# Optimization experiments

Measured on AMD Instinct MI355X. Metric: run time of the kernel, lower is better.

The kernel has to match this reference:

```python
import jax, jax.numpy as jnp
import numpy as np

SR = 44100
SHORT_TAU_MS = 50.0
LONG_TAU_MS = 3000.0


def ms2coef(ms, sr):
    return float(1.0 - np.exp(-2200.0 / (ms * sr)))


C_SHORT = ms2coef(SHORT_TAU_MS, SR)
C_LONG = ms2coef(LONG_TAU_MS, SR)
ALIGN_SHIFT = int(SR * (LONG_TAU_MS - SHORT_TAU_MS) * 0.0005)  # 65047


def _ema(x, coef):
    """One-pole EMA along last axis: y[t] = coef*x[t] + (1-coef)*y[t-1], y[-1]=0.
    Implemented as a parallel (associative) scan over the linear recurrence."""
    a = jnp.full_like(x, 1.0 - coef)
    b = coef * x

    def combine(l, r):
        a1, b1 = l
        a2, b2 = r
        return (a1 * a2, a2 * b1 + b2)

    _, y = jax.lax.associative_scan(combine, (a, b), axis=-1)
    return y


def _ldr(x):
    # flatten leading dims, then log(short EMA) - log(rolled long EMA)
    x = x.reshape(-1, x.shape[-1])
    short = _ema(x, C_SHORT)
    long_ = jnp.roll(_ema(x, C_LONG), -ALIGN_SHIFT, axis=-1)
    return jnp.log(short) - jnp.log(long_)


def setup_inputs() -> dict:
    key = jax.random.key(0)
    k1, k2 = jax.random.split(key)
    B, T = 16, 1048576
    # squared signals: strictly positive (tiny offset avoids log(0) at t=0)
    pred_sq = jax.random.uniform(k1, (B, T), dtype=jnp.float32) + 1e-6
    target_sq = jax.random.uniform(k2, (B, T), dtype=jnp.float32) + 1e-6
    return {"pred_sq": pred_sq, "target_sq": target_sq}


def reference(pred_sq, target_sq):
    return jnp.mean(jnp.abs(_ldr(pred_sq) - _ldr(target_sq)))
```

## Files before the change

kernel.cpp:

```cpp
#include <hip/hip_runtime.h>
#include <math.h>

#define TPB   256
#define SL    16
#define SEGS  65536
#define TLEN  1048576
#define MOFF  4065
#define ROFF  7
#define NEMA  4
#define TPL   256

typedef float v4f __attribute__((ext_vector_type(4)));

__device__ __forceinline__ float comp(const float4& v, int m) {
    return m == 0 ? v.x : m == 1 ? v.y : m == 2 ? v.z : v.w;
}

__device__ __forceinline__ float ipowf(float base, int e) {
    float r = 1.0f, p = base;
    while (e) { if (e & 1) r *= p; p *= p; e >>= 1; }
    return r;
}

__global__ __launch_bounds__(TPB) void ldr_partials(
    const float* __restrict__ pred, const float* __restrict__ targ,
    float amS, float amL, float Ac16S, float Ac16L,
    float* __restrict__ pB, float* __restrict__ tA, int rows)
{
    __shared__ float wt[4][NEMA];
    const int bgl = blockIdx.x;
    const int r = bgl >> 8, tile = bgl & 255;
    const int j = threadIdx.x, lane = j & 63, w = j >> 6;
    const int m = tile * 256 + j;
    const size_t base = (size_t)r * TLEN + (size_t)m * SL;
    const float* P = pred + base;
    const float* T = targ + base;

    v4f u0, u1, u2, u3, w0, w1, w2, w3;
    asm volatile(
        "global_load_dwordx4 %[u0], %[pa], off\n\t"
        "global_load_dwordx4 %[u1], %[pa], off offset:16\n\t"
        "global_load_dwordx4 %[u2], %[pa], off offset:32\n\t"
        "global_load_dwordx4 %[u3], %[pa], off offset:48\n\t"
        "global_load_dwordx4 %[w0], %[ta], off\n\t"
        "global_load_dwordx4 %[w1], %[ta], off offset:16\n\t"
        "global_load_dwordx4 %[w2], %[ta], off offset:32\n\t"
        "global_load_dwordx4 %[w3], %[ta], off offset:48\n\t"
        "s_waitcnt vmcnt(0)"
        : [u0] "=&v"(u0), [u1] "=&v"(u1), [u2] "=&v"(u2), [u3] "=&v"(u3),
          [w0] "=&v"(w0), [w1] "=&v"(w1), [w2] "=&v"(w2), [w3] "=&v"(w3)
        : [pa] "v"(P), [ta] "v"(T)
        : "memory");

    float sp = 0.f, st = 0.f, lp = 0.f, lt = 0.f;
    #define PQ(Q) { sp = fmaf(amS, sp, Q.x); lp = fmaf(amL, lp, Q.x);         \
                    sp = fmaf(amS, sp, Q.y); lp = fmaf(amL, lp, Q.y);         \
                    sp = fmaf(amS, sp, Q.z); lp = fmaf(amL, lp, Q.z);         \
                    sp = fmaf(amS, sp, Q.w); lp = fmaf(amL, lp, Q.w); }
    #define TQ(Q) { st = fmaf(amS, st, Q.x); lt = fmaf(amL, lt, Q.x);         \
                    st = fmaf(amS, st, Q.y); lt = fmaf(amL, lt, Q.y);         \
                    st = fmaf(amS, st, Q.z); lt = fmaf(amL, lt, Q.z);         \
                    st = fmaf(amS, st, Q.w); lt = fmaf(amL, lt, Q.w); }
    PQ(u0) PQ(u1) PQ(u2) PQ(u3)
    TQ(w0) TQ(w1) TQ(w2) TQ(w3)
    #undef PQ
    #undef TQ

    const size_t plane = (size_t)rows * SEGS;
    const size_t idx = (size_t)r * SEGS + m;
    pB[0 * plane + idx] = sp;
    pB[1 * plane + idx] = st;
    pB[2 * plane + idx] = lp;
    pB[3 * plane + idx] = lt;

    const float wgtS = ipowf(Ac16S, 63 - lane);
    const float wgtL = ipowf(Ac16L, 63 - lane);
    float vals[NEMA] = { sp * wgtS, st * wgtS, lp * wgtL, lt * wgtL };
    #pragma unroll
    for (int E = 0; E < NEMA; ++E) {
        float s = vals[E];
        #pragma unroll
        for (int d = 32; d > 0; d >>= 1) s += __shfl_xor(s, d, 64);
        if (lane == 0) wt[w][E] = s;
    }
    __syncthreads();
    if (j == 0) {
        const float A64S = ipowf(Ac16S, 64), A64L = ipowf(Ac16L, 64);
        #pragma unroll
        for (int E = 0; E < NEMA; ++E) {
            const float A64 = (E < 2) ? A64S : A64L;
            float t = wt[0][E];
            t = fmaf(A64, t, wt[1][E]);
            t = fmaf(A64, t, wt[2][E]);
            t = fmaf(A64, t, wt[3][E]);
            tA[((size_t)E * rows + r) * TPL + tile] = t;
        }
    }
}

__global__ __launch_bounds__(64) void ldr_tile_scan(
    const float* __restrict__ tA, float* __restrict__ tC,
    float AcT_S, float AcT_L, int rows)
{
    const int g = blockIdx.x, lane = threadIdx.x;
    const float AcT = (g < 2 * rows) ? AcT_S : AcT_L;
    const float AcT4 = ((AcT * AcT) * (AcT * AcT));
    const float* Bv = tA + (size_t)g * TPL + lane * 4;
    float b4[4];
    float B = 0.f;
    #pragma unroll
    for (int m = 0; m < 4; ++m) { b4[m] = Bv[m]; B = fmaf(AcT, B, b4[m]); }
    float incl = B, Ad = AcT4;
    #pragma unroll
    for (int d = 1; d < 64; d <<= 1) {
        float pb = __shfl_up(incl, d, 64);
        if (lane >= d) incl = fmaf(Ad, pb, incl);
        Ad *= Ad;
    }
    float carry = __shfl_up(incl, 1, 64);
    if (lane == 0) carry = 0.f;
    float* co = tC + (size_t)g * TPL + lane * 4;
    #pragma unroll
    for (int m = 0; m < 4; ++m) {
        co[m] = carry;
        carry = fmaf(AcT, carry, b4[m]);
    }
}

__global__ __launch_bounds__(TPB) void ldr_loss(
    const float* __restrict__ pred, const float* __restrict__ targ,
    const float* __restrict__ pB, const float* __restrict__ tC,
    float amS, float amL, float Ac16S, float Ac16L,
    float* __restrict__ partial, int rows)
{
    __shared__ float sS[2][4], sL[2][4];
    __shared__ float longC[2][512];
    __shared__ float rs[4];
    const int bgl = blockIdx.x;
    const int r = bgl >> 8, bl = bgl & 255;
    const int j = threadIdx.x, lane = j & 63, w = j >> 6;
    const int m = bl * 256 + j;
    const size_t plane = (size_t)rows * SEGS;
    const size_t rbase = (size_t)r * SEGS;

    const float A1024S = ipowf(Ac16S, 64);
    const float aLaneS = ipowf(Ac16S, lane);
    float aggS[2];
    aggS[0] = pB[0 * plane + rbase + m];
    aggS[1] = pB[1 * plane + rbase + m];
    float inS0 = aggS[0], inS1 = aggS[1], Ad = Ac16S;
    #pragma unroll
    for (int d = 1; d < 64; d <<= 1) {
        float p0 = __shfl_up(inS0, d, 64);
        float p1 = __shfl_up(inS1, d, 64);
        if (lane >= d) { inS0 = fmaf(Ad, p0, inS0); inS1 = fmaf(Ad, p1, inS1); }
        Ad *= Ad;
    }
    float exS0 = __shfl_up(inS0, 1, 64), exS1 = __shfl_up(inS1, 1, 64);
    if (lane == 0) { exS0 = 0.f; exS1 = 0.f; }
    if (lane == 63) { sS[0][w] = inS0; sS[1][w] = inS1; }

    const int half = j >> 7;
    const int hh = j & 127;
    const int tsel = (bl + 15 + half) & 255;
    const float Ac32L = Ac16L * Ac16L;
    const float A2048L = ipowf(Ac32L, 64);
    const float aLaneL = ipowf(Ac32L, lane);
    float2 agL0 = *(const float2*)(pB + 2 * plane + rbase + tsel * 256 + 2 * hh);
    float2 agL1 = *(const float2*)(pB + 3 * plane + rbase + tsel * 256 + 2 * hh);
    float pa0 = fmaf(Ac16L, agL0.x, agL0.y);
    float pa1 = fmaf(Ac16L, agL1.x, agL1.y);
    float inL0 = pa0, inL1 = pa1;
    Ad = Ac32L;
    #pragma unroll
    for (int d = 1; d < 64; d <<= 1) {
        float p0 = __shfl_up(inL0, d, 64);
        float p1 = __shfl_up(inL1, d, 64);
        if (lane >= d) { inL0 = fmaf(Ad, p0, inL0); inL1 = fmaf(Ad, p1, inL1); }
        Ad *= Ad;
    }
    float exL0 = __shfl_up(inL0, 1, 64), exL1 = __shfl_up(inL1, 1, 64);
    if (lane == 0) { exL0 = 0.f; exL1 = 0.f; }
    if (lane == 63) { sL[0][w] = inL0; sL[1][w] = inL1; }
    __syncthreads();

    {
        const float baseS0 = tC[((size_t)0 * rows + r) * TPL + bl];
        const float baseS1 = tC[((size_t)1 * rows + r) * TPL + bl];
        float Wc0 = 0.f, Wc1 = 0.f;
        for (int u = 0; u < w; ++u) {
            Wc0 = fmaf(Wc0, A1024S, sS[0][u]);
            Wc1 = fmaf(Wc1, A1024S, sS[1][u]);
        }
        const float aThS = aLaneS * ipowf(A1024S, w);
        exS0 = fmaf(aThS, baseS0, fmaf(aLaneS, Wc0, exS0));
        exS1 = fmaf(aThS, baseS1, fmaf(aLaneS, Wc1, exS1));
    }
    {
        const float baseL0 = tC[((size_t)2 * rows + r) * TPL + tsel];
        const float baseL1 = tC[((size_t)3 * rows + r) * TPL + tsel];
        const int hw = w & 1, fw = w & 2;
        float Wc0 = hw ? sL[0][fw] : 0.f;
        float Wc1 = hw ? sL[1][fw] : 0.f;
        const float aThL = aLaneL * (hw ? A2048L : 1.f);
        float c00 = fmaf(aThL, baseL0, fmaf(aLaneL, Wc0, exL0));
        float c10 = fmaf(aThL, baseL1, fmaf(aLaneL, Wc1, exL1));
        const int i0 = half * 256 + 2 * hh;
        longC[0][i0] = c00; longC[0][i0 + 1] = fmaf(Ac16L, c00, agL0.x);
        longC[1][i0] = c10; longC[1][i0 + 1] = fmaf(Ac16L, c10, agL1.x);
    }
    __syncthreads();
    const float cSp = exS0, cSt = exS1;
    const float cLp = longC[0][225 + j];
    const float cLt = longC[1][225 + j];

    const int a = (m + MOFF) & (SEGS - 1);
    const int bseg = (m + MOFF + 1) & (SEGS - 1);
    const float* P = pred + (size_t)r * TLEN;
    const float* T = targ + (size_t)r * TLEN;

    float sp[SL], st[SL];
    {
        const float4* Sp4 = (const float4*)(P + (size_t)m * SL);
        const float4* St4 = (const float4*)(T + (size_t)m * SL);
        float ysp = cSp, yst = cSt;
        #pragma unroll
        for (int q = 0; q < SL / 4; ++q) {
            float4 u = Sp4[q], v = St4[q];
            #pragma unroll
            for (int mm = 0; mm < 4; ++mm) {
                ysp = fmaf(amS, ysp, comp(u, mm)); sp[4 * q + mm] = ysp;
                yst = fmaf(amS, yst, comp(v, mm)); st[4 * q + mm] = yst;
            }
        }
    }
    float ylp = cLp, ylt = cLt;
    const float4* Ap4 = (const float4*)(P + (size_t)a * SL);
    const float4* At4 = (const float4*)(T + (size_t)a * SL);
    const float4* Bp4 = (const float4*)(P + (size_t)bseg * SL);
    const float4* Bt4 = (const float4*)(T + (size_t)bseg * SL);

    float lsum = 0.f;
    #pragma unroll
    for (int q = 0; q < SL / 4; ++q) {
        float4 u = Ap4[q], v = At4[q];
        #pragma unroll
        for (int mm = 0; mm < 4; ++mm) {
            const int e = 4 * q + mm;
            ylp = fmaf(amL, ylp, comp(u, mm));
            ylt = fmaf(amL, ylt, comp(v, mm));
            if (e >= ROFF) {
                const int i = e - ROFF;
                lsum += fabsf(__logf(__fdividef(sp[i] * ylt, st[i] * ylp)));
            }
        }
    }
    #pragma unroll
    for (int q = 0; q < 2; ++q) {
        float4 u = Bp4[q], v = Bt4[q];
        #pragma unroll
        for (int mm = 0; mm < 4; ++mm) {
            const int e = 4 * q + mm;
            if (e < ROFF) {
                ylp = fmaf(amL, ylp, comp(u, mm));
                ylt = fmaf(amL, ylt, comp(v, mm));
                const int i = e + (SL - ROFF);
                lsum += fabsf(__logf(__fdividef(sp[i] * ylt, st[i] * ylp)));
            }
        }
    }

    #pragma unroll
    for (int d = 32; d > 0; d >>= 1) lsum += __shfl_xor(lsum, d, 64);
    if (lane == 0) rs[w] = lsum;
    __syncthreads();
    if (j == 0) partial[bgl] = rs[0] + rs[1] + rs[2] + rs[3];
}

__global__ void ldr_finalize(const float* __restrict__ partial, int nparts,
                             float* __restrict__ out, double inv_n)
{
    __shared__ double sd[256];
    double s = 0.0;
    for (int i = threadIdx.x; i < nparts; i += 256) s += (double)partial[i];
    sd[threadIdx.x] = s;
    __syncthreads();
    for (int d = 128; d > 0; d >>= 1) {
        if (threadIdx.x < d) sd[threadIdx.x] += sd[threadIdx.x + d];
        __syncthreads();
    }
    if (threadIdx.x == 0) out[0] = (float)(sd[0] * inv_n);
}

extern "C" void kernel_launch(void* const* d_in, const int* in_sizes, int n_in,
                              void* d_out, int out_size, void* d_ws, size_t ws_size,
                              hipStream_t stream)
{
    const float* pred = (const float*)d_in[0];
    const float* targ = (const float*)d_in[1];
    const int n = in_sizes[0];
    const int rows = n / TLEN;

    const double csd = 1.0 - exp(-2200.0 / (50.0 * 44100.0));
    const double cld = 1.0 - exp(-2200.0 / (3000.0 * 44100.0));
    const double amSd = 1.0 - csd, amLd = 1.0 - cld;
    const float amS = (float)amSd, amL = (float)amLd;
    const float Ac16S = (float)pow(amSd, 16.0);
    const float Ac16L = (float)pow(amLd, 16.0);
    const float AcT_S = (float)pow(amSd, 4096.0);
    const float AcT_L = (float)pow(amLd, 4096.0);

    char* wsb = (char*)d_ws;
    float* pB      = (float*)(wsb + 256);
    float* tA      = pB + (size_t)NEMA * rows * SEGS;
    float* tC      = tA + (size_t)NEMA * rows * TPL;
    float* partial = tC + (size_t)NEMA * rows * TPL;

    const int nblocks = rows * TPL;
    const int nplanes = NEMA * rows;

    ldr_partials<<<nblocks, TPB, 0, stream>>>(pred, targ, amS, amL,
                                              Ac16S, Ac16L, pB, tA, rows);
    ldr_tile_scan<<<nplanes, 64, 0, stream>>>(tA, tC, AcT_S, AcT_L, rows);
    ldr_loss<<<nblocks, TPB, 0, stream>>>(pred, targ, pB, tC, amS, amL,
                                          Ac16S, Ac16L, partial, rows);

    const double inv_n = 1.0 / ((double)rows * (double)TLEN);
    ldr_finalize<<<1, 256, 0, stream>>>(partial, nblocks, (float*)d_out, inv_n);
}
```

Baseline: 75.51 us.

## Fuse tile scan into loss kernel and recompute short-EMA partials locally

Removes the separate tile-scan launch: each wave of every loss block redundantly scans one of the four 256-entry tile-aggregate planes and picks out the carries it needs. Short-EMA segment partials are no longer stored by the first kernel. The loss kernel instead recomputes them from its own segment loads, which it already needed, now issued up front with inline asm. This saves one launch, the scan kernel's traffic and half the partial-plane writes and reads. In exchange every block repeats the small tile scans and holds 32 more live registers across the scan phase.

```diff
diff --git a/kernel.cpp b/kernel.cpp
--- a/kernel.cpp
+++ b/kernel.cpp
@@ -7,7 +7,6 @@
 #define TLEN  1048576
 #define MOFF  4065
 #define ROFF  7
-#define NEMA  4
 #define TPL   256
 
 typedef float v4f __attribute__((ext_vector_type(4)));
@@ -22,12 +21,28 @@
     return r;
 }
 
+#define LOAD8(P, T, U0,U1,U2,U3, W0,W1,W2,W3)                                 \
+    asm volatile(                                                             \
+        "global_load_dwordx4 %[u0], %[pa], off\n\t"                           \
+        "global_load_dwordx4 %[u1], %[pa], off offset:16\n\t"                 \
+        "global_load_dwordx4 %[u2], %[pa], off offset:32\n\t"                 \
+        "global_load_dwordx4 %[u3], %[pa], off offset:48\n\t"                 \
+        "global_load_dwordx4 %[w0], %[ta], off\n\t"                           \
+        "global_load_dwordx4 %[w1], %[ta], off offset:16\n\t"                 \
+        "global_load_dwordx4 %[w2], %[ta], off offset:32\n\t"                 \
+        "global_load_dwordx4 %[w3], %[ta], off offset:48\n\t"                 \
+        "s_waitcnt vmcnt(0)"                                                  \
+        : [u0] "=&v"(U0), [u1] "=&v"(U1), [u2] "=&v"(U2), [u3] "=&v"(U3),     \
+          [w0] "=&v"(W0), [w1] "=&v"(W1), [w2] "=&v"(W2), [w3] "=&v"(W3)      \
+        : [pa] "v"(P), [ta] "v"(T)                                            \
+        : "memory")
+
 __global__ __launch_bounds__(TPB) void ldr_partials(
     const float* __restrict__ pred, const float* __restrict__ targ,
     float amS, float amL, float Ac16S, float Ac16L,
-    float* __restrict__ pB, float* __restrict__ tA, int rows)
+    float* __restrict__ pBL, float* __restrict__ tA, int rows)
 {
-    __shared__ float wt[4][NEMA];
+    __shared__ float wt[4][4];
     const int bgl = blockIdx.x;
     const int r = bgl >> 8, tile = bgl & 255;
     const int j = threadIdx.x, lane = j & 63, w = j >> 6;
@@ -37,20 +52,7 @@
     const float* T = targ + base;
 
     v4f u0, u1, u2, u3, w0, w1, w2, w3;
-    asm volatile(
-        "global_load_dwordx4 %[u0], %[pa], off\n\t"
-        "global_load_dwordx4 %[u1], %[pa], off offset:16\n\t"
-        "global_load_dwordx4 %[u2], %[pa], off offset:32\n\t"
-        "global_load_dwordx4 %[u3], %[pa], off offset:48\n\t"
-        "global_load_dwordx4 %[w0], %[ta], off\n\t"
-        "global_load_dwordx4 %[w1], %[ta], off offset:16\n\t"
-        "global_load_dwordx4 %[w2], %[ta], off offset:32\n\t"
-        "global_load_dwordx4 %[w3], %[ta], off offset:48\n\t"
-        "s_waitcnt vmcnt(0)"
-        : [u0] "=&v"(u0), [u1] "=&v"(u1), [u2] "=&v"(u2), [u3] "=&v"(u3),
-          [w0] "=&v"(w0), [w1] "=&v"(w1), [w2] "=&v"(w2), [w3] "=&v"(w3)
-        : [pa] "v"(P), [ta] "v"(T)
-        : "memory");
+    LOAD8(P, T, u0, u1, u2, u3, w0, w1, w2, w3);
 
     float sp = 0.f, st = 0.f, lp = 0.f, lt = 0.f;
     #define PQ(Q) { sp = fmaf(amS, sp, Q.x); lp = fmaf(amL, lp, Q.x);         \
@@ -68,16 +70,14 @@
 
     const size_t plane = (size_t)rows * SEGS;
     const size_t idx = (size_t)r * SEGS + m;
-    pB[0 * plane + idx] = sp;
-    pB[1 * plane + idx] = st;
-    pB[2 * plane + idx] = lp;
-    pB[3 * plane + idx] = lt;
+    pBL[0 * plane + idx] = lp;
+    pBL[1 * plane + idx] = lt;
 
     const float wgtS = ipowf(Ac16S, 63 - lane);
     const float wgtL = ipowf(Ac16L, 63 - lane);
-    float vals[NEMA] = { sp * wgtS, st * wgtS, lp * wgtL, lt * wgtL };
-    #pragma unroll
-    for (int E = 0; E < NEMA; ++E) {
+    float vals[4] = { sp * wgtS, st * wgtS, lp * wgtL, lt * wgtL };
+    #pragma unroll
+    for (int E = 0; E < 4; ++E) {
         float s = vals[E];
         #pragma unroll
         for (int d = 32; d > 0; d >>= 1) s += __shfl_xor(s, d, 64);
@@ -87,7 +87,7 @@
     if (j == 0) {
         const float A64S = ipowf(Ac16S, 64), A64L = ipowf(Ac16L, 64);
         #pragma unroll
-        for (int E = 0; E < NEMA; ++E) {
+        for (int E = 0; E < 4; ++E) {
             const float A64 = (E < 2) ? A64S : A64L;
             float t = wt[0][E];
             t = fmaf(A64, t, wt[1][E]);
@@ -98,42 +98,15 @@
     }
 }
 
-__global__ __launch_bounds__(64) void ldr_tile_scan(
-    const float* __restrict__ tA, float* __restrict__ tC,
-    float AcT_S, float AcT_L, int rows)
-{
-    const int g = blockIdx.x, lane = threadIdx.x;
-    const float AcT = (g < 2 * rows) ? AcT_S : AcT_L;
-    const float AcT4 = ((AcT * AcT) * (AcT * AcT));
-    const float* Bv = tA + (size_t)g * TPL + lane * 4;
-    float b4[4];
-    float B = 0.f;
-    #pragma unroll
-    for (int m = 0; m < 4; ++m) { b4[m] = Bv[m]; B = fmaf(AcT, B, b4[m]); }
-    float incl = B, Ad = AcT4;
-    #pragma unroll
-    for (int d = 1; d < 64; d <<= 1) {
-        float pb = __shfl_up(incl, d, 64);
-        if (lane >= d) incl = fmaf(Ad, pb, incl);
-        Ad *= Ad;
-    }
-    float carry = __shfl_up(incl, 1, 64);
-    if (lane == 0) carry = 0.f;
-    float* co = tC + (size_t)g * TPL + lane * 4;
-    #pragma unroll
-    for (int m = 0; m < 4; ++m) {
-        co[m] = carry;
-        carry = fmaf(AcT, carry, b4[m]);
-    }
-}
-
 __global__ __launch_bounds__(TPB) void ldr_loss(
     const float* __restrict__ pred, const float* __restrict__ targ,
-    const float* __restrict__ pB, const float* __restrict__ tC,
+    const float* __restrict__ pBL, const float* __restrict__ tA,
     float amS, float amL, float Ac16S, float Ac16L,
+    float AcT_S, float AcT_L,
     float* __restrict__ partial, int rows)
 {
     __shared__ float sS[2][4], sL[2][4];
+    __shared__ float tcS[2], tcL2[2][2];
     __shared__ float longC[2][512];
     __shared__ float rs[4];
     const int bgl = blockIdx.x;
@@ -142,13 +115,25 @@
     const int m = bl * 256 + j;
     const size_t plane = (size_t)rows * SEGS;
     const size_t rbase = (size_t)r * SEGS;
+    const float* P = pred + (size_t)r * TLEN;
+    const float* T = targ + (size_t)r * TLEN;
+
+    const float* Pm = P + (size_t)m * SL;
+    const float* Tm = T + (size_t)m * SL;
+    v4f ur0, ur1, ur2, ur3, tr0, tr1, tr2, tr3;
+    LOAD8(Pm, Tm, ur0, ur1, ur2, ur3, tr0, tr1, tr2, tr3);
+
+    float aggS0 = 0.f, aggS1 = 0.f;
+    #define AQ(U, V) { aggS0 = fmaf(amS, aggS0, U.x); aggS1 = fmaf(amS, aggS1, V.x); \
+                       aggS0 = fmaf(amS, aggS0, U.y); aggS1 = fmaf(amS, aggS1, V.y); \
+                       aggS0 = fmaf(amS, aggS0, U.z); aggS1 = fmaf(amS, aggS1, V.z); \
+                       aggS0 = fmaf(amS, aggS0, U.w); aggS1 = fmaf(amS, aggS1, V.w); }
+    AQ(ur0, tr0) AQ(ur1, tr1) AQ(ur2, tr2) AQ(ur3, tr3)
+    #undef AQ
 
     const float A1024S = ipowf(Ac16S, 64);
     const float aLaneS = ipowf(Ac16S, lane);
-    float aggS[2];
-    aggS[0] = pB[0 * plane + rbase + m];
-    aggS[1] = pB[1 * plane + rbase + m];
-    float inS0 = aggS[0], inS1 = aggS[1], Ad = Ac16S;
+    float inS0 = aggS0, inS1 = aggS1, Ad = Ac16S;
     #pragma unroll
     for (int d = 1; d < 64; d <<= 1) {
         float p0 = __shfl_up(inS0, d, 64);
@@ -166,8 +151,8 @@
     const float Ac32L = Ac16L * Ac16L;
     const float A2048L = ipowf(Ac32L, 64);
     const float aLaneL = ipowf(Ac32L, lane);
-    float2 agL0 = *(const float2*)(pB + 2 * plane + rbase + tsel * 256 + 2 * hh);
-    float2 agL1 = *(const float2*)(pB + 3 * plane + rbase + tsel * 256 + 2 * hh);
+    float2 agL0 = *(const float2*)(pBL + 0 * plane + rbase + tsel * 256 + 2 * hh);
+    float2 agL1 = *(const float2*)(pBL + 1 * plane + rbase + tsel * 256 + 2 * hh);
     float pa0 = fmaf(Ac16L, agL0.x, agL0.y);
     float pa1 = fmaf(Ac16L, agL1.x, agL1.y);
     float inL0 = pa0, inL1 = pa1;
@@ -182,11 +167,49 @@
     float exL0 = __shfl_up(inL0, 1, 64), exL1 = __shfl_up(inL1, 1, 64);
     if (lane == 0) { exL0 = 0.f; exL1 = 0.f; }
     if (lane == 63) { sL[0][w] = inL0; sL[1][w] = inL1; }
-    __syncthreads();
 
     {
-        const float baseS0 = tC[((size_t)0 * rows + r) * TPL + bl];
-        const float baseS1 = tC[((size_t)1 * rows + r) * TPL + bl];
+        const float AcT  = (w < 2) ? AcT_S : AcT_L;
+        const float AcT4 = (AcT * AcT) * (AcT * AcT);
+        const float* Av = tA + ((size_t)w * rows + r) * TPL + lane * 4;
+        float v0 = Av[0], v1 = Av[1], v2 = Av[2], v3 = Av[3];
+        float B = v0;
+        B = fmaf(AcT, B, v1); B = fmaf(AcT, B, v2); B = fmaf(AcT, B, v3);
+        float incl = B, Ad2 = AcT4;
+        #pragma unroll
+        for (int d = 1; d < 64; d <<= 1) {
+            float pb = __shfl_up(incl, d, 64);
+            if (lane >= d) incl = fmaf(Ad2, pb, incl);
+            Ad2 *= Ad2;
+        }
+        float carry = __shfl_up(incl, 1, 64);
+        if (lane == 0) carry = 0.f;
+        const float c0 = carry;
+        const float c1 = fmaf(AcT, c0, v0);
+        const float c2 = fmaf(AcT, c1, v1);
+        const float c3 = fmaf(AcT, c2, v2);
+        if (w < 2) {
+            if (lane == (bl >> 2)) {
+                const int s = bl & 3;
+                tcS[w] = (s == 0) ? c0 : (s == 1) ? c1 : (s == 2) ? c2 : c3;
+            }
+        } else {
+            const int t0i = (bl + 15) & 255, t1i = (bl + 16) & 255;
+            if (lane == (t0i >> 2)) {
+                const int s = t0i & 3;
+                tcL2[w - 2][0] = (s == 0) ? c0 : (s == 1) ? c1 : (s == 2) ? c2 : c3;
+            }
+            if (lane == (t1i >> 2)) {
+                const int s = t1i & 3;
+                tcL2[w - 2][1] = (s == 0) ? c0 : (s == 1) ? c1 : (s == 2) ? c2 : c3;
+            }
+        }
+    }
+    __syncthreads();
+
+    {
+        const float baseS0 = tcS[0];
+        const float baseS1 = tcS[1];
         float Wc0 = 0.f, Wc1 = 0.f;
         for (int u = 0; u < w; ++u) {
             Wc0 = fmaf(Wc0, A1024S, sS[0][u]);
@@ -197,8 +220,8 @@
         exS1 = fmaf(aThS, baseS1, fmaf(aLaneS, Wc1, exS1));
     }
     {
-        const float baseL0 = tC[((size_t)2 * rows + r) * TPL + tsel];
-        const float baseL1 = tC[((size_t)3 * rows + r) * TPL + tsel];
+        const float baseL0 = tcL2[0][half];
+        const float baseL1 = tcL2[1][half];
         const int hw = w & 1, fw = w & 2;
         float Wc0 = hw ? sL[0][fw] : 0.f;
         float Wc1 = hw ? sL[1][fw] : 0.f;
@@ -214,26 +237,24 @@
     const float cLp = longC[0][225 + j];
     const float cLt = longC[1][225 + j];
 
+    float sp[SL], st[SL];
+    {
+        float ysp = cSp, yst = cSt;
+        #define SQ(U, V, QO)                                                  \
+            { ysp = fmaf(amS, ysp, U.x); sp[QO + 0] = ysp;                    \
+              yst = fmaf(amS, yst, V.x); st[QO + 0] = yst;                    \
+              ysp = fmaf(amS, ysp, U.y); sp[QO + 1] = ysp;                    \
+              yst = fmaf(amS, yst, V.y); st[QO + 1] = yst;                    \
+              ysp = fmaf(amS, ysp, U.z); sp[QO + 2] = ysp;                    \
+              yst = fmaf(amS, yst, V.z); st[QO + 2] = yst;                    \
+              ysp = fmaf(amS, ysp, U.w); sp[QO + 3] = ysp;                    \
+              yst = fmaf(amS, yst, V.w); st[QO + 3] = yst; }
+        SQ(ur0, tr0, 0) SQ(ur1, tr1, 4) SQ(ur2, tr2, 8) SQ(ur3, tr3, 12)
+        #undef SQ
+    }
+
     const int a = (m + MOFF) & (SEGS - 1);
     const int bseg = (m + MOFF + 1) & (SEGS - 1);
-    const float* P = pred + (size_t)r * TLEN;
-    const float* T = targ + (size_t)r * TLEN;
-
-    float sp[SL], st[SL];
-    {
-        const float4* Sp4 = (const float4*)(P + (size_t)m * SL);
-        const float4* St4 = (const float4*)(T + (size_t)m * SL);
-        float ysp = cSp, yst = cSt;
-        #pragma unroll
-        for (int q = 0; q < SL / 4; ++q) {
-            float4 u = Sp4[q], v = St4[q];
-            #pragma unroll
-            for (int mm = 0; mm < 4; ++mm) {
-                ysp = fmaf(amS, ysp, comp(u, mm)); sp[4 * q + mm] = ysp;
-                yst = fmaf(amS, yst, comp(v, mm)); st[4 * q + mm] = yst;
-            }
-        }
-    }
     float ylp = cLp, ylt = cLt;
     const float4* Ap4 = (const float4*)(P + (size_t)a * SL);
     const float4* At4 = (const float4*)(T + (size_t)a * SL);
@@ -311,19 +332,17 @@
     const float AcT_L = (float)pow(amLd, 4096.0);
 
     char* wsb = (char*)d_ws;
-    float* pB      = (float*)(wsb + 256);
-    float* tA      = pB + (size_t)NEMA * rows * SEGS;
-    float* tC      = tA + (size_t)NEMA * rows * TPL;
-    float* partial = tC + (size_t)NEMA * rows * TPL;
+    float* pBL     = (float*)(wsb + 256);
+    float* tA      = pBL + (size_t)2 * rows * SEGS;
+    float* partial = tA + (size_t)4 * rows * TPL;
 
     const int nblocks = rows * TPL;
-    const int nplanes = NEMA * rows;
 
     ldr_partials<<<nblocks, TPB, 0, stream>>>(pred, targ, amS, amL,
-                                              Ac16S, Ac16L, pB, tA, rows);
-    ldr_tile_scan<<<nplanes, 64, 0, stream>>>(tA, tC, AcT_S, AcT_L, rows);
-    ldr_loss<<<nblocks, TPB, 0, stream>>>(pred, targ, pB, tC, amS, amL,
-                                          Ac16S, Ac16L, partial, rows);
+                                              Ac16S, Ac16L, pBL, tA, rows);
+    ldr_loss<<<nblocks, TPB, 0, stream>>>(pred, targ, pBL, tA, amS, amL,
+                                          Ac16S, Ac16L, AcT_S, AcT_L,
+                                          partial, rows);
 
     const double inv_n = 1.0 / ((double)rows * (double)TLEN);
     ldr_finalize<<<1, 256, 0, stream>>>(partial, nblocks, (float*)d_out, inv_n);
```

Result: no change. 76.23 us (+1.0%).
